# Kernel tuning notes

Hardware: AMD Instinct MI355X
Metric: run time of the kernel (lower is better)

## Reference

```python
import jax, jax.numpy as jnp
import numpy as np

LN_EPS = 1e-5

def _layer_norm(h, g, b):
    mu = jnp.mean(h, axis=-1, keepdims=True)
    var = jnp.mean(jnp.square(h - mu), axis=-1, keepdims=True)
    return (h - mu) * jax.lax.rsqrt(var + LN_EPS) * g + b

def _glp(x, w1, b1, g, be, w2, b2, src, dst, n_nodes):
    # per-node MLP: Linear -> LayerNorm -> ReLU -> Linear (back to in_channels)
    h = jnp.einsum('nc,ch->nh', x, w1) + b1
    h = jax.nn.relu(_layer_norm(h, g, be))
    h = jnp.einsum('nh,hc->nc', h, w2) + b2
    # scatter-max aggregation: message x_j = h[src], aggregated at dst; empty -> 0 (PyG fill)
    agg = jax.ops.segment_max(h[src], dst, num_segments=n_nodes)
    agg = jnp.where(jnp.isneginf(agg), 0.0, agg)
    return jnp.concatenate([h, agg], axis=1)

def setup_inputs() -> dict:
    key = jax.random.key(0)
    N, E, C, H, NC = 50000, 800000, 64, 64, 5000
    ks = jax.random.split(key, 24)
    inp = {
        'x': jax.random.normal(ks[0], (N, C), dtype=jnp.float32),
        'edge_index': jax.random.randint(ks[1], (2, E), 0, N, dtype=jnp.int64),
        'cluster': jax.random.randint(ks[2], (N,), 0, NC, dtype=jnp.int64),
        'batch': jnp.zeros((N,), dtype=jnp.int64),
        'n_clusters': NC,
    }
    cin = C
    ki = 3
    for i in range(3):  # in_channels doubles each layer
        inp[f'w1_{i}'] = jax.random.normal(ks[ki], (cin, H), dtype=jnp.float32) * (1.0 / np.sqrt(cin)); ki += 1
        inp[f'b1_{i}'] = jnp.zeros((H,), dtype=jnp.float32)
        inp[f'g_{i}'] = jnp.ones((H,), dtype=jnp.float32)
        inp[f'be_{i}'] = jnp.zeros((H,), dtype=jnp.float32)
        inp[f'w2_{i}'] = jax.random.normal(ks[ki], (H, cin), dtype=jnp.float32) * (1.0 / np.sqrt(H)); ki += 1
        inp[f'b2_{i}'] = jnp.zeros((cin,), dtype=jnp.float32)
        cin *= 2
    return inp

def reference(x, edge_index, cluster, batch, n_clusters,
              w1_0, b1_0, g_0, be_0, w2_0, b2_0,
              w1_1, b1_1, g_1, be_1, w2_1, b2_1,
              w1_2, b1_2, g_2, be_2, w2_2, b2_2):
    n_nodes = x.shape[0]
    src, dst = edge_index[0], edge_index[1]
    params = [(w1_0, b1_0, g_0, be_0, w2_0, b2_0),
              (w1_1, b1_1, g_1, be_1, w2_1, b2_1),
              (w1_2, b1_2, g_2, be_2, w2_2, b2_2)]
    for p in params:
        x = _glp(x, *p, src, dst, n_nodes)
    # max_pool_x(cluster, x, batch)[0]: per-cluster max over node features
    pooled = jax.ops.segment_max(x, cluster, num_segments=n_clusters)
    pooled = jnp.where(jnp.isneginf(pooled), 0.0, pooled)
    # out / out.norm(dim=0): per-feature-column L2 normalization
    return pooled / jnp.linalg.norm(pooled, axis=0)
```

## Files before the change

### kernel.cpp

```cpp
#include <hip/hip_runtime.h>
#include <hip/hip_fp16.h>

typedef unsigned short ushort_t;
typedef unsigned int uint_t;
typedef _Float16 f16_t;
typedef __attribute__((ext_vector_type(8))) _Float16 f16x8;
typedef __attribute__((ext_vector_type(4))) float f32x4;

__device__ __forceinline__ float2 h2f2(uint_t u) {
  __half2 h = *reinterpret_cast<__half2*>(&u);
  return __half22float2(h);
}
__device__ __forceinline__ uint_t f2h2(float a, float b) {
  __half2 h = __floats2half2_rn(a, b);
  return *reinterpret_cast<uint_t*>(&h);
}

template <int RSIZE, int NR>
__global__ __launch_bounds__(256) void k_cnt(const int* __restrict__ key, int* __restrict__ cnt,
                                             int n, int slen) {
  __shared__ int h[RSIZE];
  const int s = blockIdx.x / NR, r = blockIdx.x % NR;
  const int base = r * RSIZE;
  for (int i = threadIdx.x; i < RSIZE; i += 256) h[i] = 0;
  __syncthreads();
  const int i0 = s * slen, i1 = min(n, i0 + slen);
  for (int i = i0 + threadIdx.x * 4; i < i1; i += 1024) {
    int4 k4;
    if (i + 3 < i1) {
      k4 = *reinterpret_cast<const int4*>(&key[i]);
    } else {
      k4.x = key[i];
      k4.y = (i + 1 < i1) ? key[i + 1] : -1;
      k4.z = (i + 2 < i1) ? key[i + 2] : -1;
      k4.w = (i + 3 < i1) ? key[i + 3] : -1;
    }
    int d;
    d = k4.x - base; if ((unsigned)d < (unsigned)RSIZE) atomicAdd(&h[d], 1);
    d = k4.y - base; if ((unsigned)d < (unsigned)RSIZE) atomicAdd(&h[d], 1);
    d = k4.z - base; if ((unsigned)d < (unsigned)RSIZE) atomicAdd(&h[d], 1);
    d = k4.w - base; if ((unsigned)d < (unsigned)RSIZE) atomicAdd(&h[d], 1);
  }
  __syncthreads();
  const int NB = RSIZE * NR;
  for (int i = threadIdx.x; i < RSIZE; i += 256) cnt[(size_t)s * NB + base + i] = h[i];
}

__global__ void k_combine(int* __restrict__ cnt, int* __restrict__ deg, int nb, int nslice) {
  int d = blockIdx.x * 256 + threadIdx.x;
  if (d >= nb) return;
  int acc = 0;
  for (int s = 0; s < nslice; s++) {
    int c = cnt[(size_t)s * nb + d];
    cnt[(size_t)s * nb + d] = acc;
    acc += c;
  }
  deg[d] = acc;
}

__global__ __launch_bounds__(1024) void k_scan1(const int* __restrict__ deg, int* __restrict__ rowptr,
                                                int* __restrict__ blksum, int n) {
  __shared__ int wtot[16];
  const int tid = threadIdx.x, lane = tid & 63, w = tid >> 6;
  const int i = blockIdx.x * 1024 + tid;
  int v = (i < n) ? deg[i] : 0;
  int incl = v;
#pragma unroll
  for (int off = 1; off < 64; off <<= 1) {
    int t = __shfl_up(incl, off, 64);
    if (lane >= off) incl += t;
  }
  if (lane == 63) wtot[w] = incl;
  __syncthreads();
  if (w == 0) {
    int tv = (lane < 16) ? wtot[lane] : 0;
#pragma unroll
    for (int off = 1; off < 16; off <<= 1) {
      int t = __shfl_up(tv, off, 64);
      if (lane >= off) tv += t;
    }
    if (lane < 16) wtot[lane] = tv;
  }
  __syncthreads();
  int out = (w ? wtot[w - 1] : 0) + incl;
  if (i < n) rowptr[i + 1] = out;
  if (tid == 1023) blksum[blockIdx.x] = out;
}

__global__ __launch_bounds__(64) void k_scan2(int* __restrict__ blksum, int nb) {
  const int lane = threadIdx.x;
  int v = (lane < nb) ? blksum[lane] : 0;
  int incl = v;
#pragma unroll
  for (int off = 1; off < 64; off <<= 1) {
    int t = __shfl_up(incl, off, 64);
    if (lane >= off) incl += t;
  }
  if (lane < nb) blksum[lane] = incl - v;
}

__global__ __launch_bounds__(1024) void k_scan3(int* __restrict__ rowptr, const int* __restrict__ blkoff, int n) {
  const int i = blockIdx.x * 1024 + threadIdx.x;
  if (i == 0) rowptr[0] = 0;
  if (i < n) rowptr[i + 1] += blkoff[blockIdx.x];
}

template <int RSIZE, int NR, bool IDENT>
__global__ __launch_bounds__(256) void k_scat(const int* __restrict__ key, const int* __restrict__ val,
                                              const int* __restrict__ rowptr, const int* __restrict__ cnt,
                                              int* __restrict__ col, int n, int slen) {
  __shared__ int h[RSIZE];
  const int s = blockIdx.x / NR, r = blockIdx.x % NR;
  const int base = r * RSIZE;
  for (int i = threadIdx.x; i < RSIZE; i += 256) h[i] = 0;
  __syncthreads();
  const int NB = RSIZE * NR;
  const int i0 = s * slen, i1 = min(n, i0 + slen);
  for (int i = i0 + threadIdx.x * 4; i < i1; i += 1024) {
    int4 k4, v4;
    if (i + 3 < i1) {
      k4 = *reinterpret_cast<const int4*>(&key[i]);
      if (!IDENT) v4 = *reinterpret_cast<const int4*>(&val[i]);
    } else {
      k4.x = key[i];
      k4.y = (i + 1 < i1) ? key[i + 1] : -1;
      k4.z = (i + 2 < i1) ? key[i + 2] : -1;
      k4.w = (i + 3 < i1) ? key[i + 3] : -1;
      if (!IDENT) {
        v4.x = val[i];
        v4.y = (i + 1 < i1) ? val[i + 1] : 0;
        v4.z = (i + 2 < i1) ? val[i + 2] : 0;
        v4.w = (i + 3 < i1) ? val[i + 3] : 0;
      }
    }
    const int ks[4] = {k4.x, k4.y, k4.z, k4.w};
    const int vs[4] = {IDENT ? i : v4.x, IDENT ? i + 1 : v4.y, IDENT ? i + 2 : v4.z, IDENT ? i + 3 : v4.w};
#pragma unroll
    for (int u = 0; u < 4; u++) {
      int d = ks[u];
      int dr = d - base;
      if ((unsigned)dr < (unsigned)RSIZE) {
        int lr = atomicAdd(&h[dr], 1);
        int pos = rowptr[d] + cnt[(size_t)s * NB + d] + lr;
        col[pos] = vs[u];
      }
    }
  }
}

template <int CIN>
__global__ void k_prep(const float* __restrict__ w1, const float* __restrict__ w2,
                       f16_t* __restrict__ w1t_hi, f16_t* __restrict__ w1t_lo,
                       f16_t* __restrict__ w2t_hi, f16_t* __restrict__ w2t_lo) {
  int i = blockIdx.x * blockDim.x + threadIdx.x;
  const int n1 = CIN * 64;
  if (i < n1) {
    int k = i >> 6, c = i & 63;
    float v = w1[i];
    f16_t hi = (f16_t)v;
    w1t_hi[(size_t)c * CIN + k] = hi;
    w1t_lo[(size_t)c * CIN + k] = (f16_t)(v - (float)hi);
  } else if (i < 2 * n1) {
    int i2 = i - n1;
    int c = i2 / CIN, j = i2 & (CIN - 1);
    float v = w2[i2];
    f16_t hi = (f16_t)v;
    w2t_hi[(size_t)j * 64 + c] = hi;
    w2t_lo[(size_t)j * 64 + c] = (f16_t)(v - (float)hi);
  }
}

template <int CIN, typename TIN>
__global__ __launch_bounds__(256) void k_mlp(const TIN* __restrict__ xin,
                                             const f16_t* __restrict__ w1t_hi, const f16_t* __restrict__ w1t_lo,
                                             const float* __restrict__ b1, const float* __restrict__ g,
                                             const float* __restrict__ be,
                                             const f16_t* __restrict__ w2t_hi, const f16_t* __restrict__ w2t_lo,
                                             const float* __restrict__ b2,
                                             ushort_t* __restrict__ xout, int N) {
  constexpr int KC = CIN / 64;
  __shared__ __align__(16) f16_t sB[2][4096];
  __shared__ __align__(16) f16_t sX[2][4096];
  __shared__ __align__(16) f16_t sH[2][4096];

  const int tid = threadIdx.x;
  const int wave = tid >> 6, lane = tid & 63;
  const int b = lane & 15, q = lane >> 4;
  const int nb = blockIdx.x * 64;
  const int nbW = nb + wave * 16;

  f32x4 acc1[4] = {};

  for (int kc = 0; kc < KC; kc++) {
    __syncthreads();
#pragma unroll
    for (int half = 0; half < 2; half++) {
      int i = tid * 8 + half * 2048;
      int c = i >> 6, kk = i & 63;
      int t = c >> 4, bb = c & 15, kt = kk >> 5, qq = (kk >> 3) & 3;
      int dst = ((t * 2 + kt) * 64 + qq * 16 + bb) * 8;
      size_t src = (size_t)c * CIN + kc * 64 + kk;
      *reinterpret_cast<f16x8*>(&sB[0][dst]) = *reinterpret_cast<const f16x8*>(&w1t_hi[src]);
      *reinterpret_cast<f16x8*>(&sB[1][dst]) = *reinterpret_cast<const f16x8*>(&w1t_lo[src]);
    }
#pragma unroll
    for (int half = 0; half < 2; half++) {
      int i = tid * 8 + half * 2048;
      int n = i >> 6, kk = i & 63;
      int w = n >> 4, bb = n & 15, kt = kk >> 5, qq = (kk >> 3) & 3;
      int dst = ((w * 2 + kt) * 64 + qq * 16 + bb) * 8;
      int gn = nb + n;
      if (gn >= N) gn = N - 1;
      if constexpr (sizeof(TIN) == 4) {
        float f[8];
        *reinterpret_cast<float4*>(&f[0]) = *reinterpret_cast<const float4*>(&xin[(size_t)gn * CIN + kc * 64 + kk]);
        *reinterpret_cast<float4*>(&f[4]) = *reinterpret_cast<const float4*>(&xin[(size_t)gn * CIN + kc * 64 + kk + 4]);
        f16x8 vh, vl;
#pragma unroll
        for (int j = 0; j < 8; j++) {
          f16_t hi = (f16_t)f[j];
          vh[j] = hi;
          vl[j] = (f16_t)(f[j] - (float)hi);
        }
        *reinterpret_cast<f16x8*>(&sX[0][dst]) = vh;
        *reinterpret_cast<f16x8*>(&sX[1][dst]) = vl;
      } else {
        *reinterpret_cast<f16x8*>(&sX[0][dst]) =
            *reinterpret_cast<const f16x8*>(&xin[(size_t)gn * CIN + kc * 64 + kk]);
      }
    }
    __syncthreads();
#pragma unroll
    for (int kt = 0; kt < 2; kt++) {
      f16x8 a = *reinterpret_cast<const f16x8*>(&sX[0][((wave * 2 + kt) * 64 + lane) * 8]);
      f16x8 al;
      if constexpr (sizeof(TIN) == 4)
        al = *reinterpret_cast<const f16x8*>(&sX[1][((wave * 2 + kt) * 64 + lane) * 8]);
#pragma unroll
      for (int t = 0; t < 4; t++) {
        f16x8 bh = *reinterpret_cast<const f16x8*>(&sB[0][((t * 2 + kt) * 64 + lane) * 8]);
        f16x8 bl = *reinterpret_cast<const f16x8*>(&sB[1][((t * 2 + kt) * 64 + lane) * 8]);
        acc1[t] = __builtin_amdgcn_mfma_f32_16x16x32_f16(a, bh, acc1[t], 0, 0, 0);
        acc1[t] = __builtin_amdgcn_mfma_f32_16x16x32_f16(a, bl, acc1[t], 0, 0, 0);
        if constexpr (sizeof(TIN) == 4)
          acc1[t] = __builtin_amdgcn_mfma_f32_16x16x32_f16(al, bh, acc1[t], 0, 0, 0);
      }
    }
  }

  float b1v[4], gv[4], bev[4];
#pragma unroll
  for (int t = 0; t < 4; t++) {
    b1v[t] = b1[t * 16 + b];
    gv[t] = g[t * 16 + b];
    bev[t] = be[t * 16 + b];
  }
#pragma unroll
  for (int t = 0; t < 4; t++)
#pragma unroll
    for (int r = 0; r < 4; r++) acc1[t][r] += b1v[t];

  float mu[4], vv[4], rs[4];
#pragma unroll
  for (int r = 0; r < 4; r++) mu[r] = acc1[0][r] + acc1[1][r] + acc1[2][r] + acc1[3][r];
#pragma unroll
  for (int m = 1; m < 16; m <<= 1) {
#pragma unroll
    for (int r = 0; r < 4; r++) mu[r] += __shfl_xor(mu[r], m, 64);
  }
#pragma unroll
  for (int r = 0; r < 4; r++) mu[r] *= (1.f / 64.f);
#pragma unroll
  for (int r = 0; r < 4; r++) {
    float d0 = acc1[0][r] - mu[r], d1 = acc1[1][r] - mu[r];
    float d2 = acc1[2][r] - mu[r], d3 = acc1[3][r] - mu[r];
    vv[r] = d0 * d0 + d1 * d1 + d2 * d2 + d3 * d3;
  }
#pragma unroll
  for (int m = 1; m < 16; m <<= 1) {
#pragma unroll
    for (int r = 0; r < 4; r++) vv[r] += __shfl_xor(vv[r], m, 64);
  }
#pragma unroll
  for (int r = 0; r < 4; r++) rs[r] = rsqrtf(vv[r] * (1.f / 64.f) + 1e-5f);

#pragma unroll
  for (int t = 0; t < 4; t++) {
    const int kt = t >> 1;
    const int qq = (t & 1) * 2 + (b >> 3);
    const int jj = b & 7;
#pragma unroll
    for (int r = 0; r < 4; r++) {
      float h = (acc1[t][r] - mu[r]) * rs[r] * gv[t] + bev[t];
      h = fmaxf(h, 0.f);
      f16_t hh = (f16_t)h;
      int m = q * 4 + r;
      int dst = ((wave * 2 + kt) * 64 + qq * 16 + m) * 8 + jj;
      sH[0][dst] = hh;
      sH[1][dst] = (f16_t)(h - (float)hh);
    }
  }

  f16x8 ahi[2], alo[2];
#pragma unroll
  for (int kt = 0; kt < 2; kt++) {
    ahi[kt] = *reinterpret_cast<const f16x8*>(&sH[0][((wave * 2 + kt) * 64 + lane) * 8]);
    alo[kt] = *reinterpret_cast<const f16x8*>(&sH[1][((wave * 2 + kt) * 64 + lane) * 8]);
  }

  for (int jc = 0; jc < KC; jc++) {
    __syncthreads();
#pragma unroll
    for (int half = 0; half < 2; half++) {
      int i = tid * 8 + half * 2048;
      int jjn = i >> 6, cc = i & 63;
      int t2 = jjn >> 4, bb = jjn & 15, kt = cc >> 5, qq = (cc >> 3) & 3;
      int dst = ((t2 * 2 + kt) * 64 + qq * 16 + bb) * 8;
      size_t src = (size_t)(jc * 64 + jjn) * 64 + cc;
      *reinterpret_cast<f16x8*>(&sB[0][dst]) = *reinterpret_cast<const f16x8*>(&w2t_hi[src]);
      *reinterpret_cast<f16x8*>(&sB[1][dst]) = *reinterpret_cast<const f16x8*>(&w2t_lo[src]);
    }
    __syncthreads();
#pragma unroll
    for (int t2 = 0; t2 < 4; t2++) {
      f32x4 acc = {};
#pragma unroll
      for (int kt = 0; kt < 2; kt++) {
        f16x8 bh = *reinterpret_cast<const f16x8*>(&sB[0][((t2 * 2 + kt) * 64 + lane) * 8]);
        f16x8 bl = *reinterpret_cast<const f16x8*>(&sB[1][((t2 * 2 + kt) * 64 + lane) * 8]);
        acc = __builtin_amdgcn_mfma_f32_16x16x32_f16(ahi[kt], bh, acc, 0, 0, 0);
        acc = __builtin_amdgcn_mfma_f32_16x16x32_f16(ahi[kt], bl, acc, 0, 0, 0);
        acc = __builtin_amdgcn_mfma_f32_16x16x32_f16(alo[kt], bh, acc, 0, 0, 0);
      }
      int col = jc * 64 + t2 * 16 + b;
      float b2v = b2[col];
#pragma unroll
      for (int r = 0; r < 4; r++) {
        int node = nbW + q * 4 + r;
        if (node < N) {
          __half hv = __float2half_rn(acc[r] + b2v);
          xout[(size_t)node * (2 * CIN) + col] = *reinterpret_cast<ushort_t*>(&hv);
        }
      }
    }
  }
}

template <int CIN, int UNR>
__global__ __launch_bounds__(256) void k_agg(ushort_t* __restrict__ xb, const int* __restrict__ rowptr,
                                             const int* __restrict__ col, int N) {
  constexpr int LPR = CIN / 8;
  constexpr int RPW = 64 / LPR;
  const int wid = (blockIdx.x * blockDim.x + threadIdx.x) >> 6;
  const int lane = threadIdx.x & 63;
  const int sub = lane / LPR;
  const int ll = lane % LPR;
  const int node = wid * RPW + sub;
  if (node >= N) return;
  const int beg = rowptr[node], end = rowptr[node + 1];
  float v[8];
#pragma unroll
  for (int p = 0; p < 8; p++) v[p] = -INFINITY;
  for (int e = beg; e < end; e += UNR) {
    int idx[UNR];
#pragma unroll
    for (int u = 0; u < UNR; u++) { int t = e + u; idx[u] = col[t < end ? t : e]; }
    uint4 r[UNR];
#pragma unroll
    for (int u = 0; u < UNR; u++)
      r[u] = *reinterpret_cast<const uint4*>(xb + (size_t)idx[u] * (2 * CIN) + ll * 8);
#pragma unroll
    for (int u = 0; u < UNR; u++) {
      float2 f0 = h2f2(r[u].x), f1 = h2f2(r[u].y), f2 = h2f2(r[u].z), f3 = h2f2(r[u].w);
      v[0] = fmaxf(v[0], f0.x); v[1] = fmaxf(v[1], f0.y);
      v[2] = fmaxf(v[2], f1.x); v[3] = fmaxf(v[3], f1.y);
      v[4] = fmaxf(v[4], f2.x); v[5] = fmaxf(v[5], f2.y);
      v[6] = fmaxf(v[6], f3.x); v[7] = fmaxf(v[7], f3.y);
    }
  }
  if (beg == end) {
#pragma unroll
    for (int p = 0; p < 8; p++) v[p] = 0.f;
  }
  *reinterpret_cast<uint4*>(xb + (size_t)node * (2 * CIN) + CIN + ll * 8) =
      make_uint4(f2h2(v[0], v[1]), f2h2(v[2], v[3]), f2h2(v[4], v[5]), f2h2(v[6], v[7]));
}

__global__ __launch_bounds__(256) void k_pool(const ushort_t* __restrict__ x3, const int* __restrict__ rowptr,
                                              const int* __restrict__ col, float* __restrict__ pooled, int NC) {
  const int wid = (blockIdx.x * blockDim.x + threadIdx.x) >> 6;
  const int lane = threadIdx.x & 63;
  if (wid >= NC) return;
  const int beg = rowptr[wid], end = rowptr[wid + 1];
  float v[8];
#pragma unroll
  for (int p = 0; p < 8; p++) v[p] = -INFINITY;
  for (int e = beg; e < end; e += 4) {
    int idx[4];
#pragma unroll
    for (int u = 0; u < 4; u++) { int t = e + u; idx[u] = col[t < end ? t : e]; }
    uint4 r[4];
#pragma unroll
    for (int u = 0; u < 4; u++)
      r[u] = *reinterpret_cast<const uint4*>(x3 + (size_t)idx[u] * 512 + lane * 8);
#pragma unroll
    for (int u = 0; u < 4; u++) {
      float2 f0 = h2f2(r[u].x), f1 = h2f2(r[u].y), f2 = h2f2(r[u].z), f3 = h2f2(r[u].w);
      v[0] = fmaxf(v[0], f0.x); v[1] = fmaxf(v[1], f0.y);
      v[2] = fmaxf(v[2], f1.x); v[3] = fmaxf(v[3], f1.y);
      v[4] = fmaxf(v[4], f2.x); v[5] = fmaxf(v[5], f2.y);
      v[6] = fmaxf(v[6], f3.x); v[7] = fmaxf(v[7], f3.y);
    }
  }
  if (beg == end) {
#pragma unroll
    for (int p = 0; p < 8; p++) v[p] = 0.f;
  }
  float4* o = reinterpret_cast<float4*>(pooled + (size_t)wid * 512 + lane * 8);
  o[0] = make_float4(v[0], v[1], v[2], v[3]);
  o[1] = make_float4(v[4], v[5], v[6], v[7]);
}

__global__ __launch_bounds__(256) void k_norm(const float* __restrict__ pooled, float* __restrict__ normsq, int NC) {
  const int c0 = threadIdx.x;
  const int c1 = threadIdx.x + 256;
  const int rows = (NC + gridDim.x - 1) / gridDim.x;
  float s0 = 0.f, s1 = 0.f;
  for (int rr = 0; rr < rows; rr++) {
    int r = blockIdx.x * rows + rr;
    if (r < NC) {
      float v0 = pooled[(size_t)r * 512 + c0];
      float v1 = pooled[(size_t)r * 512 + c1];
      s0 = fmaf(v0, v0, s0);
      s1 = fmaf(v1, v1, s1);
    }
  }
  atomicAdd(&normsq[c0], s0);
  atomicAdd(&normsq[c1], s1);
}

__global__ void k_final(const float* __restrict__ pooled, const float* __restrict__ normsq,
                        float* __restrict__ out, int n) {
  int i = blockIdx.x * blockDim.x + threadIdx.x;
  if (i >= n) return;
  int c = i & 511;
  out[i] = pooled[i] * rsqrtf(normsq[c]);
}

extern "C" void kernel_launch(void* const* d_in, const int* in_sizes, int n_in,
                              void* d_out, int out_size, void* d_ws, size_t ws_size,
                              hipStream_t stream) {
  const int N = in_sizes[0] / 64;
  const int E = in_sizes[1] / 2;
  const int NC = out_size / 512;

  const float* x0 = (const float*)d_in[0];
  const int* ei = (const int*)d_in[1];
  const int* cluster = (const int*)d_in[2];

  const float* W[18];
  for (int k = 0; k < 18; k++) W[k] = (const float*)d_in[5 + k];

  constexpr int RSZ_E = 12544, NR_E = 4, NSL_E = 128;
  constexpr int RSZ_C = 5120, NR_C = 1, NSL_C = 32;
  const int NB_E = RSZ_E * NR_E;
  const int NB_C = RSZ_C * NR_C;
  const int slenE = (((E + NSL_E - 1) / NSL_E) + 3) & ~3;
  const int slenC = (((N + NSL_C - 1) / NSL_C) + 3) & ~3;

  char* p = (char*)d_ws;
  auto alloc = [&](size_t bytes) -> void* {
    void* r = (void*)p;
    p += (bytes + 255) & ~(size_t)255;
    return r;
  };
  ushort_t* x1h = (ushort_t*)alloc((size_t)N * 128 * 2);
  ushort_t* x2h = (ushort_t*)alloc((size_t)N * 256 * 2);
  ushort_t* x3h = (ushort_t*)alloc((size_t)N * 512 * 2);
  float* pooled = (float*)alloc((size_t)NC * 512 * 4);
  float* normsq = (float*)alloc((size_t)512 * 4);
  int* degE     = (int*)alloc((size_t)NB_E * 4);
  int* rowptrE  = (int*)alloc((size_t)(NB_E + 1) * 4);
  int* colE     = (int*)alloc((size_t)E * 4);
  int* cntE     = (int*)alloc((size_t)NSL_E * NB_E * 4);
  int* degC     = (int*)alloc((size_t)NB_C * 4);
  int* rowptrC  = (int*)alloc((size_t)(NB_C + 1) * 4);
  int* colC     = (int*)alloc((size_t)N * 4);
  int* cntC     = (int*)alloc((size_t)NSL_C * NB_C * 4);
  int* blkE     = (int*)alloc(64 * 4);
  int* blkC     = (int*)alloc(64 * 4);
  f16_t* wt[3][4];
  for (int L = 0; L < 3; L++) {
    int cin = 64 << L;
    for (int j = 0; j < 4; j++) wt[L][j] = (f16_t*)alloc((size_t)cin * 64 * 2);
  }

  hipMemsetAsync(normsq, 0, (size_t)512 * 4, stream);

  k_prep<64><<<(2 * 64 * 64 + 255) / 256, 256, 0, stream>>>(W[0], W[4], wt[0][0], wt[0][1], wt[0][2], wt[0][3]);
  k_prep<128><<<(2 * 128 * 64 + 255) / 256, 256, 0, stream>>>(W[6], W[10], wt[1][0], wt[1][1], wt[1][2], wt[1][3]);
  k_prep<256><<<(2 * 256 * 64 + 255) / 256, 256, 0, stream>>>(W[12], W[16], wt[2][0], wt[2][1], wt[2][2], wt[2][3]);

  k_cnt<RSZ_E, NR_E><<<NSL_E * NR_E, 256, 0, stream>>>(ei + E, cntE, E, slenE);
  k_combine<<<(NB_E + 255) / 256, 256, 0, stream>>>(cntE, degE, NB_E, NSL_E);
  { int nbk = (NB_E + 1023) / 1024;
    k_scan1<<<nbk, 1024, 0, stream>>>(degE, rowptrE, blkE, NB_E);
    k_scan2<<<1, 64, 0, stream>>>(blkE, nbk);
    k_scan3<<<nbk, 1024, 0, stream>>>(rowptrE, blkE, NB_E); }
  k_scat<RSZ_E, NR_E, false><<<NSL_E * NR_E, 256, 0, stream>>>(ei + E, ei, rowptrE, cntE, colE, E, slenE);

  k_cnt<RSZ_C, NR_C><<<NSL_C * NR_C, 256, 0, stream>>>(cluster, cntC, N, slenC);
  k_combine<<<(NB_C + 255) / 256, 256, 0, stream>>>(cntC, degC, NB_C, NSL_C);
  { int nbk = (NB_C + 1023) / 1024;
    k_scan1<<<nbk, 1024, 0, stream>>>(degC, rowptrC, blkC, NB_C);
    k_scan2<<<1, 64, 0, stream>>>(blkC, nbk);
    k_scan3<<<nbk, 1024, 0, stream>>>(rowptrC, blkC, NB_C); }
  k_scat<RSZ_C, NR_C, true><<<NSL_C * NR_C, 256, 0, stream>>>(cluster, nullptr, rowptrC, cntC, colC, N, slenC);

  const int nblk = (N + 63) / 64;
  k_mlp<64, float><<<nblk, 256, 0, stream>>>(x0, wt[0][0], wt[0][1], W[1], W[2], W[3],
                                             wt[0][2], wt[0][3], W[5], x1h, N);
  { int waves = (N + 7) / 8; k_agg<64, 4><<<(waves * 64 + 255) / 256, 256, 0, stream>>>(x1h, rowptrE, colE, N); }
  k_mlp<128, ushort_t><<<nblk, 256, 0, stream>>>(x1h, wt[1][0], wt[1][1], W[7], W[8], W[9],
                                                 wt[1][2], wt[1][3], W[11], x2h, N);
  { int waves = (N + 3) / 4; k_agg<128, 8><<<(waves * 64 + 255) / 256, 256, 0, stream>>>(x2h, rowptrE, colE, N); }
  k_mlp<256, ushort_t><<<nblk, 256, 0, stream>>>(x2h, wt[2][0], wt[2][1], W[13], W[14], W[15],
                                                 wt[2][2], wt[2][3], W[17], x3h, N);
  { int waves = (N + 1) / 2; k_agg<256, 8><<<(waves * 64 + 255) / 256, 256, 0, stream>>>(x3h, rowptrE, colE, N); }

  k_pool<<<(NC * 64 + 255) / 256, 256, 0, stream>>>(x3h, rowptrC, colC, pooled, NC);
  k_norm<<<128, 256, 0, stream>>>(pooled, normsq, NC);
  k_final<<<(NC * 512 + 255) / 256, 256, 0, stream>>>(pooled, normsq, (float*)d_out, NC * 512);
}
```

Measured before the change: 410.0 us.

## Fuse neighbor max-aggregation into next MLP's input load and merge prep/scan kernels

Instead of materializing the aggregated half of each layer's output in a separate k_agg pass, the next layer's MLP computes the scatter-max over neighbors on the fly while loading its input tile, so layer outputs store only the MLP half. The per-cluster count combine and scan become a single one-block kernel, the three weight-prep launches merge into one, scan2 is folded into scan3, and the pool loop unrolls by 8. The aim is to cut memory traffic and launch count. The trade-off is that the gather latency now sits inside the MLP's load phase and is recomputed per k-chunk, which can stall the MFMA work.

```diff
diff --git a/kernel.cpp b/kernel.cpp
--- a/kernel.cpp
+++ b/kernel.cpp
@@ -87,22 +87,62 @@
   if (tid == 1023) blksum[blockIdx.x] = out;
 }
 
-__global__ __launch_bounds__(64) void k_scan2(int* __restrict__ blksum, int nb) {
-  const int lane = threadIdx.x;
-  int v = (lane < nb) ? blksum[lane] : 0;
-  int incl = v;
-#pragma unroll
-  for (int off = 1; off < 64; off <<= 1) {
-    int t = __shfl_up(incl, off, 64);
-    if (lane >= off) incl += t;
-  }
-  if (lane < nb) blksum[lane] = incl - v;
-}
-
-__global__ __launch_bounds__(1024) void k_scan3(int* __restrict__ rowptr, const int* __restrict__ blkoff, int n) {
+__global__ __launch_bounds__(1024) void k_scan3(int* __restrict__ rowptr, const int* __restrict__ blksum, int n) {
+  __shared__ int soff;
+  if (threadIdx.x < 64) {
+    int v = ((int)threadIdx.x < (int)blockIdx.x) ? blksum[threadIdx.x] : 0;
+#pragma unroll
+    for (int m = 1; m < 64; m <<= 1) v += __shfl_xor(v, m, 64);
+    if (threadIdx.x == 0) soff = v;
+  }
+  __syncthreads();
   const int i = blockIdx.x * 1024 + threadIdx.x;
   if (i == 0) rowptr[0] = 0;
-  if (i < n) rowptr[i + 1] += blkoff[blockIdx.x];
+  if (i < n) rowptr[i + 1] += soff;
+}
+
+template <int NB>
+__global__ __launch_bounds__(1024) void k_combscan(int* __restrict__ cnt, int* __restrict__ rowptr, int nslice) {
+  __shared__ int sdeg[NB];
+  __shared__ int wtot[16];
+  const int tid = threadIdx.x, lane = tid & 63, w = tid >> 6;
+  for (int d = tid; d < NB; d += 1024) {
+    int acc = 0;
+    for (int s = 0; s < nslice; s++) {
+      int c = cnt[(size_t)s * NB + d];
+      cnt[(size_t)s * NB + d] = acc;
+      acc += c;
+    }
+    sdeg[d] = acc;
+  }
+  if (tid == 0) rowptr[0] = 0;
+  __syncthreads();
+  int carry = 0;
+  for (int base = 0; base < NB; base += 1024) {
+    int v = sdeg[base + tid];
+    int incl = v;
+#pragma unroll
+    for (int off = 1; off < 64; off <<= 1) {
+      int t = __shfl_up(incl, off, 64);
+      if (lane >= off) incl += t;
+    }
+    if (lane == 63) wtot[w] = incl;
+    __syncthreads();
+    if (w == 0) {
+      int tv = (lane < 16) ? wtot[lane] : 0;
+#pragma unroll
+      for (int off = 1; off < 16; off <<= 1) {
+        int t = __shfl_up(tv, off, 64);
+        if (lane >= off) tv += t;
+      }
+      if (lane < 16) wtot[lane] = tv;
+    }
+    __syncthreads();
+    int out = carry + (w ? wtot[w - 1] : 0) + incl;
+    rowptr[base + tid + 1] = out;
+    carry += wtot[15];
+    __syncthreads();
+  }
 }
 
 template <int RSIZE, int NR, bool IDENT>
@@ -148,30 +188,40 @@
   }
 }
 
-template <int CIN>
-__global__ void k_prep(const float* __restrict__ w1, const float* __restrict__ w2,
-                       f16_t* __restrict__ w1t_hi, f16_t* __restrict__ w1t_lo,
-                       f16_t* __restrict__ w2t_hi, f16_t* __restrict__ w2t_lo) {
-  int i = blockIdx.x * blockDim.x + threadIdx.x;
-  const int n1 = CIN * 64;
-  if (i < n1) {
-    int k = i >> 6, c = i & 63;
-    float v = w1[i];
+struct PrepArgs {
+  const float* w1[3];
+  const float* w2[3];
+  f16_t* o[3][4];
+};
+__global__ void k_prep_all(PrepArgs a) {
+  int i = blockIdx.x * 256 + threadIdx.x;
+  int L, base;
+  if (i < 8192) { L = 0; base = 0; }
+  else if (i < 24576) { L = 1; base = 8192; }
+  else if (i < 57344) { L = 2; base = 24576; }
+  else return;
+  const int cin = 64 << L;
+  const int n1 = cin * 64;
+  int j = i - base;
+  if (j < n1) {
+    int k = j >> 6, c = j & 63;
+    float v = a.w1[L][j];
     f16_t hi = (f16_t)v;
-    w1t_hi[(size_t)c * CIN + k] = hi;
-    w1t_lo[(size_t)c * CIN + k] = (f16_t)(v - (float)hi);
-  } else if (i < 2 * n1) {
-    int i2 = i - n1;
-    int c = i2 / CIN, j = i2 & (CIN - 1);
-    float v = w2[i2];
+    a.o[L][0][(size_t)c * cin + k] = hi;
+    a.o[L][1][(size_t)c * cin + k] = (f16_t)(v - (float)hi);
+  } else {
+    int i2 = j - n1;
+    int c = i2 / cin, jj = i2 & (cin - 1);
+    float v = a.w2[L][i2];
     f16_t hi = (f16_t)v;
-    w2t_hi[(size_t)j * 64 + c] = hi;
-    w2t_lo[(size_t)j * 64 + c] = (f16_t)(v - (float)hi);
-  }
-}
-
-template <int CIN, typename TIN>
+    a.o[L][2][(size_t)jj * 64 + c] = hi;
+    a.o[L][3][(size_t)jj * 64 + c] = (f16_t)(v - (float)hi);
+  }
+}
+
+template <int CIN, int KCH, int SOUT, typename TIN>
 __global__ __launch_bounds__(256) void k_mlp(const TIN* __restrict__ xin,
+                                             const int* __restrict__ rowptr, const int* __restrict__ col,
                                              const f16_t* __restrict__ w1t_hi, const f16_t* __restrict__ w1t_lo,
                                              const float* __restrict__ b1, const float* __restrict__ g,
                                              const float* __restrict__ be,
@@ -179,6 +229,7 @@
                                              const float* __restrict__ b2,
                                              ushort_t* __restrict__ xout, int N) {
   constexpr int KC = CIN / 64;
+  constexpr int SIN = KCH * 64;
   __shared__ __align__(16) f16_t sB[2][4096];
   __shared__ __align__(16) f16_t sX[2][4096];
   __shared__ __align__(16) f16_t sH[2][4096];
@@ -213,8 +264,8 @@
       if (gn >= N) gn = N - 1;
       if constexpr (sizeof(TIN) == 4) {
         float f[8];
-        *reinterpret_cast<float4*>(&f[0]) = *reinterpret_cast<const float4*>(&xin[(size_t)gn * CIN + kc * 64 + kk]);
-        *reinterpret_cast<float4*>(&f[4]) = *reinterpret_cast<const float4*>(&xin[(size_t)gn * CIN + kc * 64 + kk + 4]);
+        *reinterpret_cast<float4*>(&f[0]) = *reinterpret_cast<const float4*>(&xin[(size_t)gn * SIN + kc * 64 + kk]);
+        *reinterpret_cast<float4*>(&f[4]) = *reinterpret_cast<const float4*>(&xin[(size_t)gn * SIN + kc * 64 + kk + 4]);
         f16x8 vh, vl;
 #pragma unroll
         for (int j = 0; j < 8; j++) {
@@ -225,8 +276,39 @@
         *reinterpret_cast<f16x8*>(&sX[0][dst]) = vh;
         *reinterpret_cast<f16x8*>(&sX[1][dst]) = vl;
       } else {
-        *reinterpret_cast<f16x8*>(&sX[0][dst]) =
-            *reinterpret_cast<const f16x8*>(&xin[(size_t)gn * CIN + kc * 64 + kk]);
+        if (KCH == KC || kc < KCH) {
+          *reinterpret_cast<f16x8*>(&sX[0][dst]) =
+              *reinterpret_cast<const f16x8*>(&xin[(size_t)gn * SIN + kc * 64 + kk]);
+        } else {
+          const int c0 = (kc - KCH) * 64 + kk;
+          const int beg = rowptr[gn], end = rowptr[gn + 1];
+          float m[8];
+#pragma unroll
+          for (int p = 0; p < 8; p++) m[p] = -INFINITY;
+          for (int e = beg; e < end; e += 4) {
+            int idx[4];
+#pragma unroll
+            for (int u = 0; u < 4; u++) { int t2 = e + u; idx[u] = col[t2 < end ? t2 : e]; }
+            uint4 rr[4];
+#pragma unroll
+            for (int u = 0; u < 4; u++)
+              rr[u] = *reinterpret_cast<const uint4*>(&xin[(size_t)idx[u] * SIN + c0]);
+#pragma unroll
+            for (int u = 0; u < 4; u++) {
+              float2 f0 = h2f2(rr[u].x), f1 = h2f2(rr[u].y), f2v = h2f2(rr[u].z), f3 = h2f2(rr[u].w);
+              m[0] = fmaxf(m[0], f0.x); m[1] = fmaxf(m[1], f0.y);
+              m[2] = fmaxf(m[2], f1.x); m[3] = fmaxf(m[3], f1.y);
+              m[4] = fmaxf(m[4], f2v.x); m[5] = fmaxf(m[5], f2v.y);
+              m[6] = fmaxf(m[6], f3.x); m[7] = fmaxf(m[7], f3.y);
+            }
+          }
+          if (beg == end) {
+#pragma unroll
+            for (int p = 0; p < 8; p++) m[p] = 0.f;
+          }
+          uint4 pk = make_uint4(f2h2(m[0], m[1]), f2h2(m[2], m[3]), f2h2(m[4], m[5]), f2h2(m[6], m[7]));
+          *reinterpret_cast<uint4*>(&sX[0][dst]) = pk;
+        }
       }
     }
     __syncthreads();
@@ -332,14 +414,14 @@
         acc = __builtin_amdgcn_mfma_f32_16x16x32_f16(ahi[kt], bl, acc, 0, 0, 0);
         acc = __builtin_amdgcn_mfma_f32_16x16x32_f16(alo[kt], bh, acc, 0, 0, 0);
       }
-      int col = jc * 64 + t2 * 16 + b;
-      float b2v = b2[col];
+      int col2 = jc * 64 + t2 * 16 + b;
+      float b2v = b2[col2];
 #pragma unroll
       for (int r = 0; r < 4; r++) {
         int node = nbW + q * 4 + r;
         if (node < N) {
           __half hv = __float2half_rn(acc[r] + b2v);
-          xout[(size_t)node * (2 * CIN) + col] = *reinterpret_cast<ushort_t*>(&hv);
+          xout[(size_t)node * SOUT + col2] = *reinterpret_cast<ushort_t*>(&hv);
         }
       }
     }
@@ -395,16 +477,16 @@
   float v[8];
 #pragma unroll
   for (int p = 0; p < 8; p++) v[p] = -INFINITY;
-  for (int e = beg; e < end; e += 4) {
-    int idx[4];
-#pragma unroll
-    for (int u = 0; u < 4; u++) { int t = e + u; idx[u] = col[t < end ? t : e]; }
-    uint4 r[4];
-#pragma unroll
-    for (int u = 0; u < 4; u++)
+  for (int e = beg; e < end; e += 8) {
+    int idx[8];
+#pragma unroll
+    for (int u = 0; u < 8; u++) { int t = e + u; idx[u] = col[t < end ? t : e]; }
+    uint4 r[8];
+#pragma unroll
+    for (int u = 0; u < 8; u++)
       r[u] = *reinterpret_cast<const uint4*>(x3 + (size_t)idx[u] * 512 + lane * 8);
 #pragma unroll
-    for (int u = 0; u < 4; u++) {
+    for (int u = 0; u < 8; u++) {
       float2 f0 = h2f2(r[u].x), f1 = h2f2(r[u].y), f2 = h2f2(r[u].z), f3 = h2f2(r[u].w);
       v[0] = fmaxf(v[0], f0.x); v[1] = fmaxf(v[1], f0.y);
       v[2] = fmaxf(v[2], f1.x); v[3] = fmaxf(v[3], f1.y);
@@ -474,8 +556,8 @@
     p += (bytes + 255) & ~(size_t)255;
     return r;
   };
-  ushort_t* x1h = (ushort_t*)alloc((size_t)N * 128 * 2);
-  ushort_t* x2h = (ushort_t*)alloc((size_t)N * 256 * 2);
+  ushort_t* x1h = (ushort_t*)alloc((size_t)N * 64 * 2);
+  ushort_t* x2h = (ushort_t*)alloc((size_t)N * 128 * 2);
   ushort_t* x3h = (ushort_t*)alloc((size_t)N * 512 * 2);
   float* pooled = (float*)alloc((size_t)NC * 512 * 4);
   float* normsq = (float*)alloc((size_t)512 * 4);
@@ -483,12 +565,10 @@
   int* rowptrE  = (int*)alloc((size_t)(NB_E + 1) * 4);
   int* colE     = (int*)alloc((size_t)E * 4);
   int* cntE     = (int*)alloc((size_t)NSL_E * NB_E * 4);
-  int* degC     = (int*)alloc((size_t)NB_C * 4);
   int* rowptrC  = (int*)alloc((size_t)(NB_C + 1) * 4);
   int* colC     = (int*)alloc((size_t)N * 4);
   int* cntC     = (int*)alloc((size_t)NSL_C * NB_C * 4);
   int* blkE     = (int*)alloc(64 * 4);
-  int* blkC     = (int*)alloc(64 * 4);
   f16_t* wt[3][4];
   for (int L = 0; L < 3; L++) {
     int cin = 64 << L;
@@ -497,35 +577,35 @@
 
   hipMemsetAsync(normsq, 0, (size_t)512 * 4, stream);
 
-  k_prep<64><<<(2 * 64 * 64 + 255) / 256, 256, 0, stream>>>(W[0], W[4], wt[0][0], wt[0][1], wt[0][2], wt[0][3]);
-  k_prep<128><<<(2 * 128 * 64 + 255) / 256, 256, 0, stream>>>(W[6], W[10], wt[1][0], wt[1][1], wt[1][2], wt[1][3]);
-  k_prep<256><<<(2 * 256 * 64 + 255) / 256, 256, 0, stream>>>(W[12], W[16], wt[2][0], wt[2][1], wt[2][2], wt[2][3]);
+  PrepArgs pa;
+  pa.w1[0] = W[0]; pa.w2[0] = W[4];
+  pa.w1[1] = W[6]; pa.w2[1] = W[10];
+  pa.w1[2] = W[12]; pa.w2[2] = W[16];
+  for (int L = 0; L < 3; L++)
+    for (int j = 0; j < 4; j++) pa.o[L][j] = wt[L][j];
+  k_prep_all<<<(57344 + 255) / 256, 256, 0, stream>>>(pa);
 
   k_cnt<RSZ_E, NR_E><<<NSL_E * NR_E, 256, 0, stream>>>(ei + E, cntE, E, slenE);
   k_combine<<<(NB_E + 255) / 256, 256, 0, stream>>>(cntE, degE, NB_E, NSL_E);
   { int nbk = (NB_E + 1023) / 1024;
     k_scan1<<<nbk, 1024, 0, stream>>>(degE, rowptrE, blkE, NB_E);
-    k_scan2<<<1, 64, 0, stream>>>(blkE, nbk);
     k_scan3<<<nbk, 1024, 0, stream>>>(rowptrE, blkE, NB_E); }
   k_scat<RSZ_E, NR_E, false><<<NSL_E * NR_E, 256, 0, stream>>>(ei + E, ei, rowptrE, cntE, colE, E, slenE);
 
   k_cnt<RSZ_C, NR_C><<<NSL_C * NR_C, 256, 0, stream>>>(cluster, cntC, N, slenC);
-  k_combine<<<(NB_C + 255) / 256, 256, 0, stream>>>(cntC, degC, NB_C, NSL_C);
-  { int nbk = (NB_C + 1023) / 1024;
-    k_scan1<<<nbk, 1024, 0, stream>>>(degC, rowptrC, blkC, NB_C);
-    k_scan2<<<1, 64, 0, stream>>>(blkC, nbk);
-    k_scan3<<<nbk, 1024, 0, stream>>>(rowptrC, blkC, NB_C); }
+  k_combscan<NB_C><<<1, 1024, 0, stream>>>(cntC, rowptrC, NSL_C);
   k_scat<RSZ_C, NR_C, true><<<NSL_C * NR_C, 256, 0, stream>>>(cluster, nullptr, rowptrC, cntC, colC, N, slenC);
 
   const int nblk = (N + 63) / 64;
-  k_mlp<64, float><<<nblk, 256, 0, stream>>>(x0, wt[0][0], wt[0][1], W[1], W[2], W[3],
-                                             wt[0][2], wt[0][3], W[5], x1h, N);
-  { int waves = (N + 7) / 8; k_agg<64, 4><<<(waves * 64 + 255) / 256, 256, 0, stream>>>(x1h, rowptrE, colE, N); }
-  k_mlp<128, ushort_t><<<nblk, 256, 0, stream>>>(x1h, wt[1][0], wt[1][1], W[7], W[8], W[9],
-                                                 wt[1][2], wt[1][3], W[11], x2h, N);
-  { int waves = (N + 3) / 4; k_agg<128, 8><<<(waves * 64 + 255) / 256, 256, 0, stream>>>(x2h, rowptrE, colE, N); }
-  k_mlp<256, ushort_t><<<nblk, 256, 0, stream>>>(x2h, wt[2][0], wt[2][1], W[13], W[14], W[15],
-                                                 wt[2][2], wt[2][3], W[17], x3h, N);
+  k_mlp<64, 1, 64, float><<<nblk, 256, 0, stream>>>(x0, nullptr, nullptr,
+                                                    wt[0][0], wt[0][1], W[1], W[2], W[3],
+                                                    wt[0][2], wt[0][3], W[5], x1h, N);
+  k_mlp<128, 1, 128, ushort_t><<<nblk, 256, 0, stream>>>(x1h, rowptrE, colE,
+                                                         wt[1][0], wt[1][1], W[7], W[8], W[9],
+                                                         wt[1][2], wt[1][3], W[11], x2h, N);
+  k_mlp<256, 2, 512, ushort_t><<<nblk, 256, 0, stream>>>(x2h, rowptrE, colE,
+                                                         wt[2][0], wt[2][1], W[13], W[14], W[15],
+                                                         wt[2][2], wt[2][3], W[17], x3h, N);
   { int waves = (N + 1) / 2; k_agg<256, 8><<<(waves * 64 + 255) / 256, 256, 0, stream>>>(x3h, rowptrE, colE, N); }
 
   k_pool<<<(NC * 64 + 255) / 256, 256, 0, stream>>>(x3h, rowptrC, colC, pooled, NC);
```

Result: slower. 462.8 us (+12.9%).
